# Optimization experiments

Measured on AMD Instinct MI355X. Metric: run time of the kernel, lower is better.

Reference implementation:

```python
import jax, jax.numpy as jnp
import numpy as np

H = 1024

def setup_inputs() -> dict:
    key = jax.random.key(0)
    ks = jax.random.split(key, 7)
    s = 1.0 / np.sqrt(H)
    return {
        "hidden_states": jax.random.normal(ks[0], (4, 2048, H), dtype=jnp.float32),
        "Wq": jax.random.uniform(ks[1], (H, H), jnp.float32, -s, s),
        "bq": jax.random.uniform(ks[2], (H,), jnp.float32, -s, s),
        "Wk": jax.random.uniform(ks[3], (H, H), jnp.float32, -s, s),
        "bk": jax.random.uniform(ks[4], (H,), jnp.float32, -s, s),
        "Wv": jax.random.uniform(ks[5], (H, H), jnp.float32, -s, s),
        "bv": jax.random.uniform(ks[6], (H,), jnp.float32, -s, s),
    }

def reference(hidden_states, Wq, bq, Wk, bk, Wv, bv):
    # Linear projections (torch Linear: x @ W.T + b)
    q = hidden_states @ Wq.T + bq  # [B,S,H]
    k = hidden_states @ Wk.T + bk
    v = hidden_states @ Wv.T + bv
    # Unscaled attention
    probs = jax.nn.softmax(jnp.einsum("bqh,bkh->bqk", q, k), axis=-1)  # [B,S,S]
    attention_scores = jnp.sum(probs, axis=-2)  # [B,S] column sums
    context = jnp.einsum("bqk,bkh->bqh", probs, v)  # [B,S,H]
    return (context, attention_scores)
```

## Files before the change

### kernel.cpp

```cpp
#include <hip/hip_runtime.h>
#include <stdint.h>


typedef __attribute__((ext_vector_type(8))) short short8;
typedef __attribute__((ext_vector_type(4))) float floatx4;
typedef __attribute__((ext_vector_type(4))) unsigned short ushort4v;
typedef unsigned short u16;

__device__ __forceinline__ u16 f2bf(float f) {
  union { float f; uint32_t u; } v; v.f = f;
  uint32_t u = v.u;
  return (u16)((u + 0x7FFFu + ((u >> 16) & 1u)) >> 16);
}
__device__ __forceinline__ float bf2f(u16 h) {
  union { uint32_t u; float f; } v; v.u = ((uint32_t)h) << 16; return v.f;
}

#define AS3(p) ((__attribute__((address_space(3))) void*)(uint32_t)(uintptr_t)(p))
#define AS1(p) ((__attribute__((address_space(1))) void*)(uintptr_t)(p))

__global__ __launch_bounds__(256) void cvt_all_kernel(
    const float* __restrict__ hs, const float* __restrict__ Wq,
    const float* __restrict__ Wk, const float* __restrict__ Wv,
    u16* __restrict__ hsb, u16* __restrict__ Wb, float* __restrict__ lsum) {
  const int bx = blockIdx.x;
  const float* src;
  u16* dst;
  int i;
  if (bx < 8192) {
    i = bx * 1024 + threadIdx.x * 4;
    src = hs; dst = hsb;
  } else {
    const int idx = bx - 8192;
    const int p = idx >> 10, blk = idx & 1023;
    src = (p == 0) ? Wq : (p == 1) ? Wk : Wv;
    dst = Wb + p * 1048576;
    i = blk * 1024 + threadIdx.x * 4;
  }
  const float4 v = *(const float4*)(src + i);
  ushort4v o;
  o[0] = f2bf(v.x); o[1] = f2bf(v.y); o[2] = f2bf(v.z); o[3] = f2bf(v.w);
  *(ushort4v*)(dst + i) = o;
  if (bx == 0) {
    float4 z = {0.f, 0.f, 0.f, 0.f};
#pragma unroll
    for (int k = 0; k < 8; ++k)
      *(float4*)(lsum + threadIdx.x * 32 + k * 4) = z;
  }
}

__device__ __forceinline__ void gemm_core(const u16* __restrict__ A,
                                          const u16* __restrict__ B,
                                          int lda, int ldb, int K,
                                          u16* As, u16* Bs, floatx4 acc[4][4]) {
  const int tid  = threadIdx.x;
  const int lane = tid & 63;
  const int w    = tid >> 6;
  const int wr   = (w >> 1) * 64;
  const int wc   = (w & 1) * 64;
  const int fr   = lane & 15;
  const int quad = lane >> 4;

  const u16* pa[4];
  const u16* pb[4];
#pragma unroll
  for (int j = 0; j < 4; ++j) {
    const int q   = tid + j * 256;
    const int row = q >> 3, col = q & 7;
    const int gc  = col ^ (row & 7);
    pa[j] = A + row * lda + gc * 8;
    pb[j] = B + row * ldb + gc * 8;
  }

  for (int kk = 0; kk < K; kk += 64) {
#pragma unroll
    for (int j = 0; j < 4; ++j) {
      __builtin_amdgcn_global_load_lds(AS1(pa[j]), AS3(As + (tid + j * 256) * 8), 16, 0, 0);
      __builtin_amdgcn_global_load_lds(AS1(pb[j]), AS3(Bs + (tid + j * 256) * 8), 16, 0, 0);
      pa[j] += 64; pb[j] += 64;
    }
    __syncthreads();
#pragma unroll
    for (int ks = 0; ks < 2; ++ks) {
      const int pc = ((ks * 4 + quad) ^ (fr & 7)) * 8;
      short8 af[4], bfr[4];
#pragma unroll
      for (int i = 0; i < 4; ++i) {
        af[i]  = *(const short8*)(As + (wr + i * 16 + fr) * 64 + pc);
        bfr[i] = *(const short8*)(Bs + (wc + i * 16 + fr) * 64 + pc);
      }
#pragma unroll
      for (int mi = 0; mi < 4; ++mi)
#pragma unroll
        for (int ni = 0; ni < 4; ++ni)
          acc[mi][ni] = __builtin_amdgcn_mfma_f32_16x16x32_bf16(af[mi], bfr[ni],
                                                                acc[mi][ni], 0, 0, 0);
    }
    __syncthreads();
  }
}

__global__ __launch_bounds__(256, 3) void proj_kernel(
    const u16* __restrict__ hsb, const u16* __restrict__ Wb,
    const float* __restrict__ bq, const float* __restrict__ bk,
    const float* __restrict__ bv,
    u16* __restrict__ qo, u16* __restrict__ ko, u16* __restrict__ vt) {
  __shared__ __align__(16) u16 As[8192];
  __shared__ __align__(16) u16 Bs[8192];
  floatx4 acc[4][4];
#pragma unroll
  for (int i = 0; i < 4; ++i)
#pragma unroll
    for (int j = 0; j < 4; ++j) acc[i][j] = {0.f, 0.f, 0.f, 0.f};

  const int p  = blockIdx.z;
  const int m0 = blockIdx.x * 128;
  const int n0 = blockIdx.y * 128;
  gemm_core(hsb + m0 * 1024, Wb + p * 1048576 + n0 * 1024, 1024, 1024, 1024, As, Bs, acc);

  const float* bias = (p == 0) ? bq : (p == 1) ? bk : bv;
  const int lane = threadIdx.x & 63, w = threadIdx.x >> 6;
  const int wr = (w >> 1) * 64, wc = (w & 1) * 64;
  const int col = lane & 15, rg4 = (lane >> 4) * 4;

  if (p < 2) {
    u16* out = (p == 0) ? qo : ko;
#pragma unroll
    for (int mi = 0; mi < 4; ++mi)
#pragma unroll
      for (int ni = 0; ni < 4; ++ni) {
        const int n = n0 + wc + ni * 16 + col;
        const float bn = bias[n];
#pragma unroll
        for (int r = 0; r < 4; ++r) {
          const int m = m0 + wr + mi * 16 + rg4 + r;
          out[m * 1024 + n] = f2bf(acc[mi][ni][r] + bn);
        }
      }
  } else {
#pragma unroll
    for (int mi = 0; mi < 4; ++mi) {
      const int mbase = m0 + wr + mi * 16 + rg4;
      const int b = mbase >> 11, s = mbase & 2047;
#pragma unroll
      for (int ni = 0; ni < 4; ++ni) {
        const int n = n0 + wc + ni * 16 + col;
        const float bn = bias[n];
        ushort4v pk;
#pragma unroll
        for (int r = 0; r < 4; ++r) pk[r] = f2bf(acc[mi][ni][r] + bn);
        *(ushort4v*)(vt + b * 2097152 + n * 2048 + s) = pk;
      }
    }
  }
}

__global__ __launch_bounds__(256) void logits_kernel(
    const u16* __restrict__ q, const u16* __restrict__ k,
    u16* __restrict__ E, float* __restrict__ lsum) {
  __shared__ __align__(16) u16 As[8192];
  __shared__ __align__(16) u16 Bs[8192];
  floatx4 acc[4][4];
#pragma unroll
  for (int i = 0; i < 4; ++i)
#pragma unroll
    for (int j = 0; j < 4; ++j) acc[i][j] = {0.f, 0.f, 0.f, 0.f};

  const int b  = blockIdx.z;
  const int m0 = blockIdx.y * 128;
  const int n0 = blockIdx.x * 128;
  gemm_core(q + (b * 2048 + m0) * 1024, k + (b * 2048 + n0) * 1024,
            1024, 1024, 1024, As, Bs, acc);

  const int lane = threadIdx.x & 63, w = threadIdx.x >> 6;
  const int wr = (w >> 1) * 64, wc = (w & 1) * 64;
  const int col = lane & 15, rg4 = (lane >> 4) * 4;
  u16* Eb = E + b * 4194304;
  float* lb = lsum + b * 2048;

#pragma unroll
  for (int mi = 0; mi < 4; ++mi) {
    floatx4 rs = {0.f, 0.f, 0.f, 0.f};
    const int rbase = m0 + wr + mi * 16 + rg4;
#pragma unroll
    for (int ni = 0; ni < 4; ++ni) {
      const int n = n0 + wc + ni * 16 + col;
#pragma unroll
      for (int r = 0; r < 4; ++r) {
        const float e = __expf(acc[mi][ni][r]);
        rs[r] += e;
        Eb[(rbase + r) * 2048 + n] = f2bf(e);
      }
    }
#pragma unroll
    for (int off = 1; off < 16; off <<= 1) {
      rs[0] += __shfl_xor(rs[0], off, 64);
      rs[1] += __shfl_xor(rs[1], off, 64);
      rs[2] += __shfl_xor(rs[2], off, 64);
      rs[3] += __shfl_xor(rs[3], off, 64);
    }
    if ((lane & 15) == 0) {
#pragma unroll
      for (int r = 0; r < 4; ++r) atomicAdd(&lb[rbase + r], rs[r]);
    }
  }
}

__global__ __launch_bounds__(256, 3) void context_kernel(
    const u16* __restrict__ E, const u16* __restrict__ vt,
    const float* __restrict__ lsum, float* __restrict__ out) {
  __shared__ __align__(16) u16 As[8192];
  __shared__ __align__(16) u16 Bs[8192];
  floatx4 acc[4][4];
#pragma unroll
  for (int i = 0; i < 4; ++i)
#pragma unroll
    for (int j = 0; j < 4; ++j) acc[i][j] = {0.f, 0.f, 0.f, 0.f};

  const int b  = blockIdx.z;
  const int m0 = blockIdx.y * 128;
  const int n0 = blockIdx.x * 128;
  gemm_core(E + b * 4194304 + m0 * 2048, vt + b * 2097152 + n0 * 2048,
            2048, 2048, 2048, As, Bs, acc);

  const int lane = threadIdx.x & 63, w = threadIdx.x >> 6;
  const int wr = (w >> 1) * 64, wc = (w & 1) * 64;
  const int col = lane & 15, rg4 = (lane >> 4) * 4;
  const float* lb = lsum + b * 2048;

#pragma unroll
  for (int mi = 0; mi < 4; ++mi) {
    const int rbase = m0 + wr + mi * 16 + rg4;
    float rinv[4];
#pragma unroll
    for (int r = 0; r < 4; ++r) rinv[r] = 1.0f / lb[rbase + r];
#pragma unroll
    for (int ni = 0; ni < 4; ++ni) {
      const int n = n0 + wc + ni * 16 + col;
#pragma unroll
      for (int r = 0; r < 4; ++r)
        out[(b * 2048 + rbase + r) * 1024 + n] = acc[mi][ni][r] * rinv[r];
    }
  }
}

__global__ __launch_bounds__(256) void colsum_part_kernel(
    const u16* __restrict__ E, const float* __restrict__ lsum,
    float* __restrict__ part) {
  const int b  = blockIdx.x;
  const int g  = blockIdx.y;
  const int q0 = g * 64;
  const int j  = threadIdx.x * 8;
  const u16* Eb = E + b * 4194304;
  const float* lb = lsum + b * 2048;
  float acc[8];
#pragma unroll
  for (int c = 0; c < 8; ++c) acc[c] = 0.f;
  for (int r = 0; r < 64; ++r) {
    const int qi = q0 + r;
    const float rinv = 1.0f / lb[qi];
    const short8 ev = *(const short8*)(Eb + qi * 2048 + j);
#pragma unroll
    for (int c = 0; c < 8; ++c) acc[c] += bf2f((u16)ev[c]) * rinv;
  }
  float* pb = part + (b * 32 + g) * 2048 + j;
#pragma unroll
  for (int c = 0; c < 8; ++c) pb[c] = acc[c];
}

__global__ __launch_bounds__(256) void colsum_reduce_kernel(
    const float* __restrict__ part, float* __restrict__ scores) {
  const int b = blockIdx.x;
  const int j = blockIdx.y * 256 + threadIdx.x;
  const float* pb = part + b * 32 * 2048 + j;
  float s = 0.f;
#pragma unroll
  for (int g = 0; g < 32; ++g) s += pb[g * 2048];
  scores[b * 2048 + j] = s;
}

extern "C" void kernel_launch(void* const* d_in, const int* in_sizes, int n_in,
                              void* d_out, int out_size, void* d_ws, size_t ws_size,
                              hipStream_t stream) {
  const float* hs = (const float*)d_in[0];
  const float* Wq = (const float*)d_in[1];
  const float* bq = (const float*)d_in[2];
  const float* Wk = (const float*)d_in[3];
  const float* bk = (const float*)d_in[4];
  const float* Wv = (const float*)d_in[5];
  const float* bv = (const float*)d_in[6];

  char* ws = (char*)d_ws;
  u16*   qw  = (u16*)(ws);
  u16*   kw  = (u16*)(ws + (16u << 20));
  u16*   vtw = (u16*)(ws + (32u << 20));
  float* lw  = (float*)(ws + (48u << 20));
  float* pw  = (float*)(ws + (48u << 20) + (128u << 10));
  u16*   hsb = (u16*)(ws + (49u << 20));
  u16*   Wb  = (u16*)(ws + (65u << 20));
  u16*   Ew  = (u16*)(ws + (49u << 20));

  float* outc = (float*)d_out;
  float* outs = outc + 8388608;

  cvt_all_kernel<<<11264, 256, 0, stream>>>(hs, Wq, Wk, Wv, hsb, Wb, lw);
  proj_kernel<<<dim3(64, 8, 3), 256, 0, stream>>>(hsb, Wb, bq, bk, bv, qw, kw, vtw);
  logits_kernel<<<dim3(16, 16, 4), 256, 0, stream>>>(qw, kw, Ew, lw);
  context_kernel<<<dim3(8, 16, 4), 256, 0, stream>>>(Ew, vtw, lw, outc);
  colsum_part_kernel<<<dim3(4, 32), 256, 0, stream>>>(Ew, lw, pw);
  colsum_reduce_kernel<<<dim3(4, 8), 256, 0, stream>>>(pw, outs);
}
```

Baseline: 249.5 us.

## Merge context GEMM and column-sum kernels into one launch with last-block reduction

```diff
diff --git a/kernel.cpp b/kernel.cpp
--- a/kernel.cpp
+++ b/kernel.cpp
@@ -22,7 +22,8 @@
 __global__ __launch_bounds__(256) void cvt_all_kernel(
     const float* __restrict__ hs, const float* __restrict__ Wq,
     const float* __restrict__ Wk, const float* __restrict__ Wv,
-    u16* __restrict__ hsb, u16* __restrict__ Wb, float* __restrict__ lsum) {
+    u16* __restrict__ hsb, u16* __restrict__ Wb, float* __restrict__ lsum,
+    int* __restrict__ cnt) {
   const int bx = blockIdx.x;
   const float* src;
   u16* dst;
@@ -46,6 +47,7 @@
 #pragma unroll
     for (int k = 0; k < 8; ++k)
       *(float4*)(lsum + threadIdx.x * 32 + k * 4) = z;
+    if (threadIdx.x < 4) cnt[threadIdx.x] = 0;
   }
 }
 
@@ -206,77 +208,88 @@
   }
 }
 
-__global__ __launch_bounds__(256, 3) void context_kernel(
+__global__ __launch_bounds__(256) void ctx_colsum_kernel(
     const u16* __restrict__ E, const u16* __restrict__ vt,
-    const float* __restrict__ lsum, float* __restrict__ out) {
+    const float* __restrict__ lsum, float* __restrict__ part,
+    int* __restrict__ cnt, float* __restrict__ outc, float* __restrict__ outs) {
   __shared__ __align__(16) u16 As[8192];
   __shared__ __align__(16) u16 Bs[8192];
-  floatx4 acc[4][4];
-#pragma unroll
-  for (int i = 0; i < 4; ++i)
-#pragma unroll
-    for (int j = 0; j < 4; ++j) acc[i][j] = {0.f, 0.f, 0.f, 0.f};
-
-  const int b  = blockIdx.z;
-  const int m0 = blockIdx.y * 128;
-  const int n0 = blockIdx.x * 128;
-  gemm_core(E + b * 4194304 + m0 * 2048, vt + b * 2097152 + n0 * 2048,
-            2048, 2048, 2048, As, Bs, acc);
-
-  const int lane = threadIdx.x & 63, w = threadIdx.x >> 6;
-  const int wr = (w >> 1) * 64, wc = (w & 1) * 64;
-  const int col = lane & 15, rg4 = (lane >> 4) * 4;
-  const float* lb = lsum + b * 2048;
-
-#pragma unroll
-  for (int mi = 0; mi < 4; ++mi) {
-    const int rbase = m0 + wr + mi * 16 + rg4;
-    float rinv[4];
-#pragma unroll
-    for (int r = 0; r < 4; ++r) rinv[r] = 1.0f / lb[rbase + r];
-#pragma unroll
-    for (int ni = 0; ni < 4; ++ni) {
-      const int n = n0 + wc + ni * 16 + col;
-#pragma unroll
-      for (int r = 0; r < 4; ++r)
-        out[(b * 2048 + rbase + r) * 1024 + n] = acc[mi][ni][r] * rinv[r];
-    }
-  }
-}
-
-__global__ __launch_bounds__(256) void colsum_part_kernel(
-    const u16* __restrict__ E, const float* __restrict__ lsum,
-    float* __restrict__ part) {
-  const int b  = blockIdx.x;
-  const int g  = blockIdx.y;
-  const int q0 = g * 64;
-  const int j  = threadIdx.x * 8;
-  const u16* Eb = E + b * 4194304;
-  const float* lb = lsum + b * 2048;
-  float acc[8];
-#pragma unroll
-  for (int c = 0; c < 8; ++c) acc[c] = 0.f;
-  for (int r = 0; r < 64; ++r) {
-    const int qi = q0 + r;
-    const float rinv = 1.0f / lb[qi];
-    const short8 ev = *(const short8*)(Eb + qi * 2048 + j);
-#pragma unroll
-    for (int c = 0; c < 8; ++c) acc[c] += bf2f((u16)ev[c]) * rinv;
-  }
-  float* pb = part + (b * 32 + g) * 2048 + j;
-#pragma unroll
-  for (int c = 0; c < 8; ++c) pb[c] = acc[c];
-}
-
-__global__ __launch_bounds__(256) void colsum_reduce_kernel(
-    const float* __restrict__ part, float* __restrict__ scores) {
-  const int b = blockIdx.x;
-  const int j = blockIdx.y * 256 + threadIdx.x;
-  const float* pb = part + b * 32 * 2048 + j;
-  float s = 0.f;
-#pragma unroll
-  for (int g = 0; g < 32; ++g) s += pb[g * 2048];
-  scores[b * 2048 + j] = s;
+  const int bid = blockIdx.x;
+
+  if (bid < 512) {
+    floatx4 acc[4][4];
+#pragma unroll
+    for (int i = 0; i < 4; ++i)
+#pragma unroll
+      for (int j = 0; j < 4; ++j) acc[i][j] = {0.f, 0.f, 0.f, 0.f};
+
+    const int b  = bid >> 7;
+    const int m0 = ((bid >> 3) & 15) * 128;
+    const int n0 = (bid & 7) * 128;
+    gemm_core(E + b * 4194304 + m0 * 2048, vt + b * 2097152 + n0 * 2048,
+              2048, 2048, 2048, As, Bs, acc);
+
+    const int lane = threadIdx.x & 63, w = threadIdx.x >> 6;
+    const int wr = (w >> 1) * 64, wc = (w & 1) * 64;
+    const int col = lane & 15, rg4 = (lane >> 4) * 4;
+    const float* lb = lsum + b * 2048;
+
+#pragma unroll
+    for (int mi = 0; mi < 4; ++mi) {
+      const int rbase = m0 + wr + mi * 16 + rg4;
+      float rinv[4];
+#pragma unroll
+      for (int r = 0; r < 4; ++r) rinv[r] = 1.0f / lb[rbase + r];
+#pragma unroll
+      for (int ni = 0; ni < 4; ++ni) {
+        const int n = n0 + wc + ni * 16 + col;
+#pragma unroll
+        for (int r = 0; r < 4; ++r)
+          outc[(b * 2048 + rbase + r) * 1024 + n] = acc[mi][ni][r] * rinv[r];
+      }
+    }
+  } else {
+    const int idx = bid - 512;
+    const int b = idx >> 5, g = idx & 31;
+    const int q0 = g * 64;
+    const int j  = threadIdx.x * 8;
+    const u16* Eb = E + b * 4194304;
+    const float* lb = lsum + b * 2048;
+    float acc[8];
+#pragma unroll
+    for (int c = 0; c < 8; ++c) acc[c] = 0.f;
+    for (int r = 0; r < 64; ++r) {
+      const int qi = q0 + r;
+      const float rinv = 1.0f / lb[qi];
+      const short8 ev = *(const short8*)(Eb + qi * 2048 + j);
+#pragma unroll
+      for (int c = 0; c < 8; ++c) acc[c] += bf2f((u16)ev[c]) * rinv;
+    }
+    float* pb = part + (b * 32 + g) * 2048 + j;
+#pragma unroll
+    for (int c = 0; c < 8; ++c) pb[c] = acc[c];
+
+    __threadfence();
+    int* sh = (int*)As;
+    if (threadIdx.x == 0) sh[0] = atomicAdd(&cnt[b], 1);
+    __syncthreads();
+    if (sh[0] == 31) {
+      __threadfence();
+      const float* pbb = part + b * 65536 + j;
+      float s[8];
+#pragma unroll
+      for (int c = 0; c < 8; ++c) s[c] = 0.f;
+#pragma unroll
+      for (int gg = 0; gg < 32; ++gg) {
+        const floatx4 v0 = *(const floatx4*)(pbb + gg * 2048);
+        const floatx4 v1 = *(const floatx4*)(pbb + gg * 2048 + 4);
+#pragma unroll
+        for (int c = 0; c < 4; ++c) { s[c] += v0[c]; s[c + 4] += v1[c]; }
+      }
+#pragma unroll
+      for (int c = 0; c < 8; ++c) outs[b * 2048 + j + c] = s[c];
+    }
+  }
 }
 
 extern "C" void kernel_launch(void* const* d_in, const int* in_sizes, int n_in,
@@ -295,6 +308,7 @@
   u16*   kw  = (u16*)(ws + (16u << 20));
   u16*   vtw = (u16*)(ws + (32u << 20));
   float* lw  = (float*)(ws + (48u << 20));
+  int*   cw  = (int*)(ws + (48u << 20) + (96u << 10));
   float* pw  = (float*)(ws + (48u << 20) + (128u << 10));
   u16*   hsb = (u16*)(ws + (49u << 20));
   u16*   Wb  = (u16*)(ws + (65u << 20));
@@ -303,10 +317,8 @@
   float* outc = (float*)d_out;
   float* outs = outc + 8388608;
 
-  cvt_all_kernel<<<11264, 256, 0, stream>>>(hs, Wq, Wk, Wv, hsb, Wb, lw);
+  cvt_all_kernel<<<11264, 256, 0, stream>>>(hs, Wq, Wk, Wv, hsb, Wb, lw, cw);
   proj_kernel<<<dim3(64, 8, 3), 256, 0, stream>>>(hsb, Wb, bq, bk, bv, qw, kw, vtw);
   logits_kernel<<<dim3(16, 16, 4), 256, 0, stream>>>(qw, kw, Ew, lw);
-  context_kernel<<<dim3(8, 16, 4), 256, 0, stream>>>(Ew, vtw, lw, outc);
-  colsum_part_kernel<<<dim3(4, 32), 256, 0, stream>>>(Ew, lw, pw);
-  colsum_reduce_kernel<<<dim3(4, 8), 256, 0, stream>>>(pw, outs);
-}
+  ctx_colsum_kernel<<<640, 256, 0, stream>>>(Ew, vtw, lw, pw, cw, outc, outs);
+}
```

After: 292.7 us. +17.3%, slower.
